# Optimization experiments

Hardware: AMD Instinct MI355X
Metric: run time of the kernel (lower is better)

The kernel has to match this reference:

```python
import jax, jax.numpy as jnp
import numpy as np

LAYERS, BLOCKS = 10, 2
RES_C, DIL_C, SKIP_C = 128, 128, 256
IN_C, COND_C, OUT_C = 60, 80, 240
INIT_K, K = 10, 2


def _dilations():
    dils = []
    for b in range(BLOCKS):
        n = LAYERS if b < BLOCKS - 1 else LAYERS - 1
        dils += [2 ** i for i in range(n)]
    return dils  # length = blocks*layers - 1 = 19


def conv1d(x, w, b, dilation=1):
    # x: [B, Cin, T], w: [Cout, Cin, K], VALID padding (no padding, like torch Conv1d default)
    y = jax.lax.conv_general_dilated(
        x, w, window_strides=(1,), padding='VALID',
        rhs_dilation=(dilation,), dimension_numbers=('NCH', 'OIH', 'NCH'))
    return y + b[None, :, None]


def setup_inputs() -> dict:
    key = jax.random.key(0)
    ks = jax.random.split(key, 18)
    L = len(_dilations())
    s = 0.05
    return {
        'input': jax.random.normal(ks[0], (4, IN_C, 6144), dtype=jnp.float32),
        'condition': jax.random.normal(ks[1], (4, COND_C, 1), dtype=jnp.float32),
        'start_w': jax.random.normal(ks[2], (RES_C, IN_C, INIT_K), dtype=jnp.float32) * s,
        'start_b': jax.random.normal(ks[3], (RES_C,), dtype=jnp.float32) * s,
        'dil_w': jax.random.normal(ks[4], (L, 2 * DIL_C, RES_C, K), dtype=jnp.float32) * s,
        'dil_b': jax.random.normal(ks[5], (L, 2 * DIL_C), dtype=jnp.float32) * s,
        'cond_w': jax.random.normal(ks[6], (L, 2 * DIL_C, COND_C, 1), dtype=jnp.float32) * s,
        'cond_b': jax.random.normal(ks[7], (L, 2 * DIL_C), dtype=jnp.float32) * s,
        'res_w': jax.random.normal(ks[8], (L, RES_C, DIL_C, 1), dtype=jnp.float32) * s,
        'res_b': jax.random.normal(ks[9], (L, RES_C), dtype=jnp.float32) * s,
        'skip_w': jax.random.normal(ks[10], (L, SKIP_C, DIL_C, 1), dtype=jnp.float32) * s,
        'skip_b': jax.random.normal(ks[11], (L, SKIP_C), dtype=jnp.float32) * s,
        'end_w': jax.random.normal(ks[12], (OUT_C, SKIP_C, 1), dtype=jnp.float32) * s,
        'end_b': jax.random.normal(ks[13], (OUT_C,), dtype=jnp.float32) * s,
        'cond_end_w': jax.random.normal(ks[14], (SKIP_C, COND_C, 1), dtype=jnp.float32) * s,
        'cond_end_b': jax.random.normal(ks[15], (SKIP_C,), dtype=jnp.float32) * s,
    }


def reference(input, condition, start_w, start_b, dil_w, dil_b, cond_w, cond_b,
              res_w, res_b, skip_w, skip_b, end_w, end_b, cond_end_w, cond_end_b):
    dils = _dilations()
    cvec = condition[:, :, 0]  # [B, cond_c] (condition time dim is 1)
    x = conv1d(input, start_w, start_b)  # [B, R, T - initK + 1]
    skip = None
    for i, d in enumerate(dils):
        residual = x
        dilated = conv1d(x, dil_w[i], dil_b[i], dilation=d)  # [B, 2C, T_i]
        condi = jnp.einsum('oc,bc->bo', cond_w[i, :, :, 0], cvec) + cond_b[i]
        dilated = dilated + condi[:, :, None]  # broadcast over time (expand)
        filt, gate = jnp.split(dilated, 2, axis=1)
        x = jnp.tanh(filt) * jax.nn.sigmoid(gate)  # [B, C, T_i]
        s = conv1d(x, skip_w[i], skip_b[i])  # [B, S, T_i]
        skip = s if skip is None else s + skip[:, :, -s.shape[2]:]
        x = conv1d(x, res_w[i], res_b[i])
        x = x + residual[:, :, -x.shape[2]:]
    cend = jnp.einsum('oc,bc->bo', cond_end_w[:, :, 0], cvec) + cond_end_b
    skip = skip + cend[:, :, None]
    out = conv1d(jnp.tanh(skip), end_w, end_b)  # [B, out_c, T_out]
    return jax.nn.sigmoid(out)  # hparams.type == 2
```

## Files before the change

kernel.cpp:

```cpp
#include <hip/hip_runtime.h>
#include <cstdint>
#include <cstddef>

#define NLAYERS 19
#define NB 4
#define RES_C 128
#define DIL2 256
#define SKIPC 256
#define INC 60
#define CONDC 80
#define OUTC 240
#define T_IN 6144
#define T0LEN 6135
#define T_FIN 4601
#define TILE 64
#define LTILE 32
#define BLK 512
#define ZROWS 4608

#define NDIL (NLAYERS*256*256)
#define NSKP (NLAYERS*256*128)
#define NRES (NLAYERS*128*128)
#define NEND (256*256)
#define NSTART (10*128*64)

typedef short bf16x8 __attribute__((ext_vector_type(8)));
typedef float f32x4 __attribute__((ext_vector_type(4)));
typedef unsigned uint32x2 __attribute__((ext_vector_type(2)));

#if __has_builtin(__builtin_amdgcn_exp2f)
#define EXP2F(x) __builtin_amdgcn_exp2f(x)
#else
#define EXP2F(x) exp2f(x)
#endif
#if __has_builtin(__builtin_amdgcn_rcpf)
#define RCPF(x) __builtin_amdgcn_rcpf(x)
#else
#define RCPF(x) (1.0f/(x))
#endif

__device__ __forceinline__ float fexp(float x){ return EXP2F(x * 1.4426950408889634f); }
__device__ __forceinline__ float fsigmoid(float x){ return RCPF(1.0f + fexp(-x)); }
__device__ __forceinline__ float ftanh(float x){ return 1.0f - 2.0f * RCPF(1.0f + fexp(2.0f*x)); }

__device__ __forceinline__ unsigned short f2bf(float f){
  unsigned u = __builtin_bit_cast(unsigned, f);
  u = u + 0x7FFFu + ((u >> 16) & 1u);
  return (unsigned short)(u >> 16);
}

__global__ void prep_weights(const float* __restrict__ dil_w, const float* __restrict__ skip_w,
                             const float* __restrict__ res_w, const float* __restrict__ end_w,
                             const float* __restrict__ start_w,
                             unsigned short* __restrict__ dilWb, unsigned short* __restrict__ skipWb,
                             unsigned short* __restrict__ resWb, unsigned short* __restrict__ endWb,
                             unsigned short* __restrict__ startWb){
  const int total = NDIL + NSKP + NRES + NEND + NSTART;
  for (int idx = blockIdx.x*256 + threadIdx.x; idx < total; idx += gridDim.x*256){
    if (idx < NDIL){
      int l = idx >> 16; int rem = idx & 65535; int m = rem >> 8; int k = rem & 255;
      int o = ((m & 1) << 7) + (m >> 1); int c = k & 127; int tap = k >> 7;
      dilWb[idx] = f2bf(dil_w[(((size_t)l*256 + o)*128 + c)*2 + tap]);
    } else if (idx < NDIL + NSKP){
      int j = idx - NDIL;
      skipWb[j] = f2bf(skip_w[j]);
    } else if (idx < NDIL + NSKP + NRES){
      int j = idx - NDIL - NSKP;
      resWb[j] = f2bf(res_w[j]);
    } else if (idx < NDIL + NSKP + NRES + NEND){
      int j = idx - NDIL - NSKP - NRES;
      int m = j >> 8; int k = j & 255;
      endWb[j] = (m < OUTC) ? f2bf(end_w[(size_t)m*256 + k]) : 0;
    } else {
      int j = idx - NDIL - NSKP - NRES - NEND;
      int k = j >> 13; int rem = j & 8191; int oc = rem >> 6; int c = rem & 63;
      startWb[j] = (c < INC) ? f2bf(start_w[((size_t)oc*INC + c)*10 + k]) : 0;
    }
  }
}

__global__ void prep_bias(const float* __restrict__ cond, const float* __restrict__ dil_b,
                          const float* __restrict__ cond_w, const float* __restrict__ cond_b,
                          const float* __restrict__ cend_w, const float* __restrict__ cend_b,
                          const float* __restrict__ skip_b,
                          float* __restrict__ cbias, float* __restrict__ sbc){
  int blk = blockIdx.x; int m = threadIdx.x;
  if (blk < NLAYERS*NB){
    int l = blk >> 2, b = blk & 3;
    int o = ((m & 1) << 7) + (m >> 1);
    float acc = dil_b[l*256 + o] + cond_b[l*256 + o];
    const float* w = cond_w + ((size_t)l*256 + o)*CONDC;
    const float* cv = cond + b*CONDC;
    for (int c = 0; c < CONDC; ++c) acc += w[c]*cv[c];
    cbias[((size_t)l*NB + b)*256 + m] = acc;
  } else {
    int b = blk - NLAYERS*NB;
    float acc = cend_b[m];
    const float* w = cend_w + (size_t)m*CONDC;
    const float* cv = cond + b*CONDC;
    for (int c = 0; c < CONDC; ++c) acc += w[c]*cv[c];
    for (int l = 0; l < NLAYERS; ++l) acc += skip_b[l*256 + m];
    sbc[b*256 + m] = acc;
  }
}

__global__ __launch_bounds__(BLK) void start_mfma(const float* __restrict__ in,
    const unsigned short* __restrict__ startWb, const float* __restrict__ bias,
    float* __restrict__ xout){
  __shared__ char Bs[80*128];
  const int tid = threadIdx.x;
  const int b = blockIdx.y; const int t0 = blockIdx.x * TILE;
  const int lane = tid & 63;
  const int wave = __builtin_amdgcn_readfirstlane(tid >> 6);
  const int q = lane >> 4, r16 = lane & 15;

  #pragma unroll
  for (int i = 0; i < 5; ++i){
    int j = tid + i*BLK;
    int c2 = j / 80, tt = j % 80;
    int c = 2*c2; int gt = t0 + tt;
    float v0 = 0.f, v1 = 0.f;
    if (gt < T_IN && c < INC){
      const float* base = in + ((size_t)(b*INC + c))*T_IN + gt;
      v0 = base[0]; v1 = base[T_IN];
    }
    unsigned u = (unsigned)f2bf(v0) | ((unsigned)f2bf(v1) << 16);
    int slot = c2 >> 2;
    *(unsigned*)(Bs + tt*128 + ((((slot ^ (tt & 7)) << 4)) | ((4*c2) & 15))) = u;
  }
  __syncthreads();

  f32x4 acc[4] = {};
  for (int k = 0; k < 10; ++k){
    const unsigned short* A = startWb + ((size_t)k*128 + wave*16)*64;
    #pragma unroll
    for (int kk = 0; kk < 2; ++kk){
      int k0 = kk*32 + q*8;
      bf16x8 a = *(const bf16x8*)(A + (size_t)r16*64 + k0);
      int slot = k0 >> 3;
      #pragma unroll
      for (int nt = 0; nt < 4; ++nt){
        int t = nt*16 + r16 + k;
        bf16x8 bf = *(const bf16x8*)(Bs + t*128 + ((slot ^ (t & 7)) << 4));
        acc[nt] = __builtin_amdgcn_mfma_f32_16x16x32_bf16(a, bf, acc[nt], 0, 0, 0);
      }
    }
  }
  const float* bb = bias + wave*16;
  #pragma unroll
  for (int nt = 0; nt < 4; ++nt){
    int gt = t0 + nt*16 + r16;
    if (gt < T0LEN){
      #pragma unroll
      for (int rr = 0; rr < 4; ++rr){
        int oc = wave*16 + 4*q + rr;
        xout[(size_t)(b*RES_C + oc)*T_IN + gt] = acc[nt][rr] + bb[4*q + rr];
      }
    }
  }
}

__global__ __launch_bounds__(BLK) void layer_mfma(
    const float* __restrict__ xin, float* __restrict__ xout,
    unsigned short* __restrict__ zl,
    const unsigned short* __restrict__ dilWb, const unsigned short* __restrict__ resWb,
    const float* __restrict__ cbias, const float* __restrict__ res_b,
    int layer, int d, int Tin, int Tout, int woff, int last){
  __shared__ char Bx[LTILE*512];
  __shared__ char Bz[LTILE*256];
  const int tid = threadIdx.x;
  const int b = blockIdx.y; const int t0 = blockIdx.x*LTILE;
  const int lane = tid & 63;
  const int wave = __builtin_amdgcn_readfirstlane(tid >> 6);
  const int q = lane >> 4;
  const int r16 = lane & 15;

  {
    const int t = lane & 31;
    const int kh = lane >> 5;
    const int gt = t0 + t;
    #pragma unroll
    for (int i = 0; i < 16; i += 2){
      int k0 = wave*32 + kh*16 + i;
      int tap = k0 >> 7; int c = k0 & 127;
      int gtt = gt + (tap ? d : 0);
      float v0 = 0.f, v1 = 0.f;
      if (gtt < Tin){
        const float* base = xin + ((size_t)(b*RES_C + c))*T_IN + gtt;
        v0 = base[0]; v1 = base[T_IN];
      }
      unsigned u = (unsigned)f2bf(v0) | ((unsigned)f2bf(v1) << 16);
      int slot = k0 >> 3;
      *(unsigned*)(Bx + t*512 + ((slot ^ (t & 31)) << 4) + ((2*k0) & 15)) = u;
    }
  }
  __syncthreads();

  f32x4 acc[2][2] = {};
  {
    const unsigned short* A = dilWb + (size_t)layer*256*256 + (size_t)(wave*32)*256;
    for (int kk = 0; kk < 8; ++kk){
      int k0 = kk*32 + q*8;
      bf16x8 a0 = *(const bf16x8*)(A + (size_t)r16*256 + k0);
      bf16x8 a1 = *(const bf16x8*)(A + (size_t)(16 + r16)*256 + k0);
      int slot = k0 >> 3;
      #pragma unroll
      for (int nt = 0; nt < 2; ++nt){
        int t = nt*16 + r16;
        bf16x8 bf = *(const bf16x8*)(Bx + t*512 + ((slot ^ (t & 31)) << 4));
        acc[0][nt] = __builtin_amdgcn_mfma_f32_16x16x32_bf16(a0, bf, acc[0][nt], 0, 0, 0);
        acc[1][nt] = __builtin_amdgcn_mfma_f32_16x16x32_bf16(a1, bf, acc[1][nt], 0, 0, 0);
      }
    }
  }

  {
    const float* cb = cbias + ((size_t)layer*NB + b)*256 + wave*32;
    #pragma unroll
    for (int mt = 0; mt < 2; ++mt){
      float bf0 = cb[mt*16 + 4*q + 0];
      float bg0 = cb[mt*16 + 4*q + 1];
      float bf1 = cb[mt*16 + 4*q + 2];
      float bg1 = cb[mt*16 + 4*q + 3];
      int ch0 = wave*16 + mt*8 + 2*q;
      int slot = ch0 >> 3;
      #pragma unroll
      for (int nt = 0; nt < 2; ++nt){
        float z0 = ftanh(acc[mt][nt][0] + bf0) * fsigmoid(acc[mt][nt][1] + bg0);
        float z1 = ftanh(acc[mt][nt][2] + bf1) * fsigmoid(acc[mt][nt][3] + bg1);
        int t = nt*16 + r16;
        unsigned u = (unsigned)f2bf(z0) | ((unsigned)f2bf(z1) << 16);
        *(unsigned*)(Bz + t*256 + ((slot ^ (t & 15)) << 4) + ((2*ch0) & 15)) = u;
      }
    }
  }
  __syncthreads();

  {
    unsigned short* zgb = zl + (size_t)b*ZROWS*128;
    #pragma unroll
    for (int i = 0; i < 4; ++i){
      int j = tid + i*BLK;
      int row = j >> 6, cu = j & 63;
      int gt = t0 + row;
      int windex = gt - woff;
      if (gt < Tout && windex >= 0){
        int slot = cu >> 2;
        unsigned u = *(const unsigned*)(Bz + row*256 + (((slot ^ (row & 15)) << 4) | ((4*cu) & 15)));
        *(unsigned*)(zgb + (size_t)windex*128 + 2*cu) = u;
      }
    }
  }

  if (!last){
    f32x4 racc[2] = {};
    const unsigned short* A = resWb + (size_t)layer*128*128 + (size_t)(wave*16)*128;
    for (int kk = 0; kk < 4; ++kk){
      int k0 = kk*32 + q*8;
      bf16x8 a0 = *(const bf16x8*)(A + (size_t)r16*128 + k0);
      int slot = k0 >> 3;
      #pragma unroll
      for (int nt = 0; nt < 2; ++nt){
        int t = nt*16 + r16;
        bf16x8 bf = *(const bf16x8*)(Bz + t*256 + ((slot ^ (t & 15)) << 4));
        racc[nt] = __builtin_amdgcn_mfma_f32_16x16x32_bf16(a0, bf, racc[nt], 0, 0, 0);
      }
    }
    const float* rb = res_b + layer*RES_C + wave*16;
    #pragma unroll
    for (int nt = 0; nt < 2; ++nt){
      int gt = t0 + nt*16 + r16;
      if (gt < Tout){
        #pragma unroll
        for (int rr = 0; rr < 4; ++rr){
          int m = wave*16 + 4*q + rr;
          size_t base = ((size_t)(b*RES_C + m))*T_IN;
          xout[base + gt] = racc[nt][rr] + rb[4*q + rr] + xin[base + gt + d];
        }
      }
    }
  }
}

__global__ __launch_bounds__(BLK) void final_mfma(
    const unsigned short* __restrict__ zbuf,
    const unsigned short* __restrict__ skipWb, const unsigned short* __restrict__ endWb,
    const float* __restrict__ sbc, const float* __restrict__ end_b,
    float* __restrict__ out){
  __shared__ char BzP[2][64*256];
  __shared__ char Bs[64*512];
  const int tid = threadIdx.x;
  const int b = blockIdx.y; const int t0 = blockIdx.x*TILE;
  const int lane = tid & 63;
  const int wave = __builtin_amdgcn_readfirstlane(tid >> 6);
  const int q = lane >> 4, r16 = lane & 15;

  auto stageZ = [&](int l, int buf){
    const unsigned* zsrc = (const unsigned*)(zbuf + (((size_t)l*NB + b)*ZROWS + t0)*128);
    char* dst = BzP[buf];
    #pragma unroll
    for (int i = 0; i < 8; ++i){
      int j = tid + i*BLK;
      int row = j >> 6, cu = j & 63;
      unsigned v = zsrc[(size_t)row*64 + cu];
      int slot = cu >> 2;
      *(unsigned*)(dst + row*256 + (((slot ^ (row & 15)) << 4) | ((4*cu) & 15))) = v;
    }
  };

  stageZ(0, 0);
  __syncthreads();

  f32x4 sacc[2][4] = {};
  for (int l = 0; l < NLAYERS; ++l){
    if (l + 1 < NLAYERS) stageZ(l + 1, (l + 1) & 1);
    const unsigned short* A = skipWb + ((size_t)l*256 + wave*32)*128;
    const char* Bb = BzP[l & 1];
    for (int kk = 0; kk < 4; ++kk){
      int k0 = kk*32 + q*8;
      bf16x8 a0 = *(const bf16x8*)(A + (size_t)r16*128 + k0);
      bf16x8 a1 = *(const bf16x8*)(A + (size_t)(16 + r16)*128 + k0);
      int slot = k0 >> 3;
      #pragma unroll
      for (int nt = 0; nt < 4; ++nt){
        int t = nt*16 + r16;
        bf16x8 bf = *(const bf16x8*)(Bb + t*256 + ((slot ^ (t & 15)) << 4));
        sacc[0][nt] = __builtin_amdgcn_mfma_f32_16x16x32_bf16(a0, bf, sacc[0][nt], 0, 0, 0);
        sacc[1][nt] = __builtin_amdgcn_mfma_f32_16x16x32_bf16(a1, bf, sacc[1][nt], 0, 0, 0);
      }
    }
    __syncthreads();
  }

  {
    const float* sb = sbc + b*256 + wave*32;
    #pragma unroll
    for (int mt = 0; mt < 2; ++mt){
      #pragma unroll
      for (int nt = 0; nt < 4; ++nt){
        int t = nt*16 + r16;
        float v0 = ftanh(sacc[mt][nt][0] + sb[mt*16 + 4*q + 0]);
        float v1 = ftanh(sacc[mt][nt][1] + sb[mt*16 + 4*q + 1]);
        float v2 = ftanh(sacc[mt][nt][2] + sb[mt*16 + 4*q + 2]);
        float v3 = ftanh(sacc[mt][nt][3] + sb[mt*16 + 4*q + 3]);
        uint32x2 u;
        u.x = (unsigned)f2bf(v0) | ((unsigned)f2bf(v1) << 16);
        u.y = (unsigned)f2bf(v2) | ((unsigned)f2bf(v3) << 16);
        int m0 = wave*32 + mt*16 + 4*q;
        int slot = (2*m0) >> 4;
        *(uint32x2*)(Bs + t*512 + (((slot ^ (t & 31)) << 4) | ((2*m0) & 15))) = u;
      }
    }
  }
  __syncthreads();

  f32x4 eacc[2][4] = {};
  const unsigned short* A = endWb + (size_t)(wave*32)*256;
  for (int kk = 0; kk < 8; ++kk){
    int k0 = kk*32 + q*8;
    bf16x8 a0 = *(const bf16x8*)(A + (size_t)r16*256 + k0);
    bf16x8 a1 = *(const bf16x8*)(A + (size_t)(16 + r16)*256 + k0);
    int slot = k0 >> 3;
    #pragma unroll
    for (int nt = 0; nt < 4; ++nt){
      int t = nt*16 + r16;
      bf16x8 bf = *(const bf16x8*)(Bs + t*512 + ((slot ^ (t & 31)) << 4));
      eacc[0][nt] = __builtin_amdgcn_mfma_f32_16x16x32_bf16(a0, bf, eacc[0][nt], 0, 0, 0);
      eacc[1][nt] = __builtin_amdgcn_mfma_f32_16x16x32_bf16(a1, bf, eacc[1][nt], 0, 0, 0);
    }
  }
  #pragma unroll
  for (int mt = 0; mt < 2; ++mt){
    #pragma unroll
    for (int nt = 0; nt < 4; ++nt){
      int gt = t0 + nt*16 + r16;
      if (gt < T_FIN){
        #pragma unroll
        for (int rr = 0; rr < 4; ++rr){
          int m = wave*32 + mt*16 + 4*q + rr;
          if (m < OUTC)
            out[((size_t)(b*OUTC + m))*T_FIN + gt] = fsigmoid(eacc[mt][nt][rr] + end_b[m]);
        }
      }
    }
  }
}

extern "C" void kernel_launch(void* const* d_in, const int* in_sizes, int n_in,
                              void* d_out, int out_size, void* d_ws, size_t ws_size,
                              hipStream_t stream){
  const float* input     = (const float*)d_in[0];
  const float* condition = (const float*)d_in[1];
  const float* start_w   = (const float*)d_in[2];
  const float* start_b   = (const float*)d_in[3];
  const float* dil_w     = (const float*)d_in[4];
  const float* dil_b     = (const float*)d_in[5];
  const float* cond_w    = (const float*)d_in[6];
  const float* cond_b    = (const float*)d_in[7];
  const float* res_w     = (const float*)d_in[8];
  const float* res_b     = (const float*)d_in[9];
  const float* skip_w    = (const float*)d_in[10];
  const float* skip_b    = (const float*)d_in[11];
  const float* end_w     = (const float*)d_in[12];
  const float* end_b     = (const float*)d_in[13];
  const float* cend_w    = (const float*)d_in[14];
  const float* cend_b    = (const float*)d_in[15];
  float* out = (float*)d_out;

  char* ws = (char*)d_ws;
  size_t off = 0;
  auto carve = [&](size_t bytes) -> char* {
    char* p = ws + off; off = (off + bytes + 255) & ~(size_t)255; return p;
  };
  float* xA            = (float*)carve((size_t)NB*RES_C*T_IN*4);
  float* xB            = (float*)carve((size_t)NB*RES_C*T_IN*4);
  unsigned short* zbuf = (unsigned short*)carve((size_t)NLAYERS*NB*ZROWS*128*2);
  unsigned short* dilWb   = (unsigned short*)carve((size_t)NDIL*2);
  unsigned short* skipWb  = (unsigned short*)carve((size_t)NSKP*2);
  unsigned short* resWb   = (unsigned short*)carve((size_t)NRES*2);
  unsigned short* endWb   = (unsigned short*)carve((size_t)NEND*2);
  unsigned short* startWb = (unsigned short*)carve((size_t)NSTART*2);
  float* cbias = (float*)carve((size_t)NLAYERS*NB*256*4);
  float* sbc   = (float*)carve((size_t)NB*256*4);

  prep_weights<<<2048, 256, 0, stream>>>(dil_w, skip_w, res_w, end_w, start_w,
                                         dilWb, skipWb, resWb, endWb, startWb);
  prep_bias<<<NLAYERS*NB + NB, 256, 0, stream>>>(condition, dil_b, cond_w, cond_b,
                                                 cend_w, cend_b, skip_b, cbias, sbc);

  {
    dim3 grid((T0LEN + TILE - 1)/TILE, NB);
    start_mfma<<<grid, BLK, 0, stream>>>(input, startWb, start_b, xA);
  }

  int dils[NLAYERS]; int n = 0;
  for (int bb = 0; bb < 2; ++bb){ int nn = (bb==0) ? 10 : 9; for (int k = 0; k < nn; ++k) dils[n++] = 1<<k; }

  float* xin = xA; float* xo = xB;
  int Tin = T0LEN;
  for (int i = 0; i < NLAYERS; ++i){
    int d = dils[i]; int Tout = Tin - d;
    dim3 grid((Tout + LTILE - 1)/LTILE, NB);
    unsigned short* zl = zbuf + (size_t)i*NB*ZROWS*128;
    layer_mfma<<<grid, BLK, 0, stream>>>(xin, xo, zl, dilWb, resWb, cbias, res_b,
                                         i, d, Tin, Tout, Tout - T_FIN,
                                         (i==NLAYERS-1)?1:0);
    float* tmp = xin; xin = xo; xo = tmp;
    Tin = Tout;
  }

  {
    dim3 grid((T_FIN + TILE - 1)/TILE, NB);
    final_mfma<<<grid, BLK, 0, stream>>>(zbuf, skipWb, endWb, sbc, end_b, out);
  }
}
```

Measured before the change: 551.8 us.

## Split skip-sum over layer groups and add separate end-conv kernel

```diff
diff --git a/kernel.cpp b/kernel.cpp
--- a/kernel.cpp
+++ b/kernel.cpp
@@ -17,6 +17,8 @@
 #define LTILE 32
 #define BLK 512
 #define ZROWS 4608
+#define NSPLIT 4
+#define LPG 5
 
 #define NDIL (NLAYERS*256*256)
 #define NSKP (NLAYERS*256*128)
@@ -175,6 +177,19 @@
   const int q = lane >> 4;
   const int r16 = lane & 15;
 
+  float resid[2][4];
+  if (!last){
+    #pragma unroll
+    for (int nt = 0; nt < 2; ++nt){
+      int gt = t0 + nt*16 + r16;
+      #pragma unroll
+      for (int rr = 0; rr < 4; ++rr){
+        int m = wave*16 + 4*q + rr;
+        resid[nt][rr] = (gt < Tout) ? xin[((size_t)(b*RES_C + m))*T_IN + gt + d] : 0.f;
+      }
+    }
+  }
+
   {
     const int t = lane & 31;
     const int kh = lane >> 5;
@@ -275,22 +290,23 @@
         for (int rr = 0; rr < 4; ++rr){
           int m = wave*16 + 4*q + rr;
           size_t base = ((size_t)(b*RES_C + m))*T_IN;
-          xout[base + gt] = racc[nt][rr] + rb[4*q + rr] + xin[base + gt + d];
+          xout[base + gt] = racc[nt][rr] + rb[4*q + rr] + resid[nt][rr];
         }
       }
     }
   }
 }
 
-__global__ __launch_bounds__(BLK) void final_mfma(
+__global__ __launch_bounds__(BLK) void skipsum_mfma(
     const unsigned short* __restrict__ zbuf,
-    const unsigned short* __restrict__ skipWb, const unsigned short* __restrict__ endWb,
-    const float* __restrict__ sbc, const float* __restrict__ end_b,
-    float* __restrict__ out){
+    const unsigned short* __restrict__ skipWb,
+    float* __restrict__ partial){
   __shared__ char BzP[2][64*256];
-  __shared__ char Bs[64*512];
   const int tid = threadIdx.x;
   const int b = blockIdx.y; const int t0 = blockIdx.x*TILE;
+  const int g = blockIdx.z;
+  const int l0 = g*LPG;
+  const int l1 = (l0 + LPG < NLAYERS) ? (l0 + LPG) : NLAYERS;
   const int lane = tid & 63;
   const int wave = __builtin_amdgcn_readfirstlane(tid >> 6);
   const int q = lane >> 4, r16 = lane & 15;
@@ -308,12 +324,12 @@
     }
   };
 
-  stageZ(0, 0);
+  stageZ(l0, l0 & 1);
   __syncthreads();
 
   f32x4 sacc[2][4] = {};
-  for (int l = 0; l < NLAYERS; ++l){
-    if (l + 1 < NLAYERS) stageZ(l + 1, (l + 1) & 1);
+  for (int l = l0; l < l1; ++l){
+    if (l + 1 < l1) stageZ(l + 1, (l + 1) & 1);
     const unsigned short* A = skipWb + ((size_t)l*256 + wave*32)*128;
     const char* Bb = BzP[l & 1];
     for (int kk = 0; kk < 4; ++kk){
@@ -332,29 +348,60 @@
     __syncthreads();
   }
 
-  {
-    const float* sb = sbc + b*256 + wave*32;
-    #pragma unroll
-    for (int mt = 0; mt < 2; ++mt){
-      #pragma unroll
-      for (int nt = 0; nt < 4; ++nt){
-        int t = nt*16 + r16;
-        float v0 = ftanh(sacc[mt][nt][0] + sb[mt*16 + 4*q + 0]);
-        float v1 = ftanh(sacc[mt][nt][1] + sb[mt*16 + 4*q + 1]);
-        float v2 = ftanh(sacc[mt][nt][2] + sb[mt*16 + 4*q + 2]);
-        float v3 = ftanh(sacc[mt][nt][3] + sb[mt*16 + 4*q + 3]);
-        uint32x2 u;
-        u.x = (unsigned)f2bf(v0) | ((unsigned)f2bf(v1) << 16);
-        u.y = (unsigned)f2bf(v2) | ((unsigned)f2bf(v3) << 16);
-        int m0 = wave*32 + mt*16 + 4*q;
-        int slot = (2*m0) >> 4;
-        *(uint32x2*)(Bs + t*512 + (((slot ^ (t & 31)) << 4) | ((2*m0) & 15))) = u;
-      }
+  float* pg = partial + (size_t)g*NB*SKIPC*T_FIN;
+  #pragma unroll
+  for (int mt = 0; mt < 2; ++mt){
+    #pragma unroll
+    for (int nt = 0; nt < 4; ++nt){
+      int gt = t0 + nt*16 + r16;
+      if (gt < T_FIN){
+        #pragma unroll
+        for (int rr = 0; rr < 4; ++rr){
+          int m = wave*32 + mt*16 + 4*q + rr;
+          pg[((size_t)(b*SKIPC + m))*T_FIN + gt] = sacc[mt][nt][rr];
+        }
+      }
+    }
+  }
+}
+
+__global__ __launch_bounds__(BLK) void end_mfma(
+    const float* __restrict__ partial, const unsigned short* __restrict__ endWb,
+    const float* __restrict__ sbc, const float* __restrict__ end_b,
+    float* __restrict__ out){
+  __shared__ char Bs[64*512];
+  const int tid = threadIdx.x;
+  const int b = blockIdx.y; const int t0 = blockIdx.x*TILE;
+  const int lane = tid & 63;
+  const int wave = __builtin_amdgcn_readfirstlane(tid >> 6);
+  const int q = lane >> 4;
+  const int r16 = lane & 15;
+  const size_t gs = (size_t)NB*SKIPC*T_FIN;
+
+  {
+    const int t = lane;
+    const int gt = t0 + t;
+    #pragma unroll
+    for (int i = 0; i < 32; i += 2){
+      int s0 = wave*32 + i;
+      float v0 = 0.f, v1 = 0.f;
+      if (gt < T_FIN){
+        size_t base = ((size_t)(b*SKIPC + s0))*T_FIN + gt;
+        float a0 = partial[base]        + partial[base + gs]
+                 + partial[base + 2*gs] + partial[base + 3*gs];
+        float a1 = partial[base + T_FIN]        + partial[base + T_FIN + gs]
+                 + partial[base + T_FIN + 2*gs] + partial[base + T_FIN + 3*gs];
+        v0 = ftanh(a0 + sbc[b*256 + s0]);
+        v1 = ftanh(a1 + sbc[b*256 + s0 + 1]);
+      }
+      unsigned u = (unsigned)f2bf(v0) | ((unsigned)f2bf(v1) << 16);
+      int slot = s0 >> 3;
+      *(unsigned*)(Bs + t*512 + ((slot ^ (t & 31)) << 4) + ((2*s0) & 15)) = u;
     }
   }
   __syncthreads();
 
-  f32x4 eacc[2][4] = {};
+  f32x4 acc[2][4] = {};
   const unsigned short* A = endWb + (size_t)(wave*32)*256;
   for (int kk = 0; kk < 8; ++kk){
     int k0 = kk*32 + q*8;
@@ -365,8 +412,8 @@
     for (int nt = 0; nt < 4; ++nt){
       int t = nt*16 + r16;
       bf16x8 bf = *(const bf16x8*)(Bs + t*512 + ((slot ^ (t & 31)) << 4));
-      eacc[0][nt] = __builtin_amdgcn_mfma_f32_16x16x32_bf16(a0, bf, eacc[0][nt], 0, 0, 0);
-      eacc[1][nt] = __builtin_amdgcn_mfma_f32_16x16x32_bf16(a1, bf, eacc[1][nt], 0, 0, 0);
+      acc[0][nt] = __builtin_amdgcn_mfma_f32_16x16x32_bf16(a0, bf, acc[0][nt], 0, 0, 0);
+      acc[1][nt] = __builtin_amdgcn_mfma_f32_16x16x32_bf16(a1, bf, acc[1][nt], 0, 0, 0);
     }
   }
   #pragma unroll
@@ -379,7 +426,7 @@
         for (int rr = 0; rr < 4; ++rr){
           int m = wave*32 + mt*16 + 4*q + rr;
           if (m < OUTC)
-            out[((size_t)(b*OUTC + m))*T_FIN + gt] = fsigmoid(eacc[mt][nt][rr] + end_b[m]);
+            out[((size_t)(b*OUTC + m))*T_FIN + gt] = fsigmoid(acc[mt][nt][rr] + end_b[m]);
         }
       }
     }
@@ -415,6 +462,7 @@
   float* xA            = (float*)carve((size_t)NB*RES_C*T_IN*4);
   float* xB            = (float*)carve((size_t)NB*RES_C*T_IN*4);
   unsigned short* zbuf = (unsigned short*)carve((size_t)NLAYERS*NB*ZROWS*128*2);
+  float* partial       = (float*)carve((size_t)NSPLIT*NB*SKIPC*T_FIN*4);
   unsigned short* dilWb   = (unsigned short*)carve((size_t)NDIL*2);
   unsigned short* skipWb  = (unsigned short*)carve((size_t)NSKP*2);
   unsigned short* resWb   = (unsigned short*)carve((size_t)NRES*2);
@@ -450,7 +498,11 @@
   }
 
   {
+    dim3 grid((T_FIN + TILE - 1)/TILE, NB, NSPLIT);
+    skipsum_mfma<<<grid, BLK, 0, stream>>>(zbuf, skipWb, partial);
+  }
+  {
     dim3 grid((T_FIN + TILE - 1)/TILE, NB);
-    final_mfma<<<grid, BLK, 0, stream>>>(zbuf, skipWb, endWb, sbc, end_b, out);
-  }
-}
+    end_mfma<<<grid, BLK, 0, stream>>>(partial, endWb, sbc, end_b, out);
+  }
+}
```

Result: no change. 556.8 us (+0.9%).
